# Kernel tuning notes

Hardware: AMD Instinct MI355X
Metric: run time of the kernel (lower is better)

## Reference

```python
import jax, jax.numpy as jnp
import numpy as np

N_CHARS, EMB, HID, T = 256, 512, 2048, 8192


def setup_inputs() -> dict:
    key = jax.random.key(0)
    ks = jax.random.split(key, 12)
    s_in = 1.0 / np.sqrt(EMB + HID)
    s_out = 1.0 / np.sqrt(HID)
    return {
        "input_seq": jax.random.randint(ks[0], (T,), 0, N_CHARS, dtype=jnp.int32),
        "emb": jax.random.normal(ks[1], (N_CHARS, EMB), jnp.float32),
        "W_f": jax.random.uniform(ks[2], (HID, EMB + HID), jnp.float32, -s_in, s_in),
        "b_f": jax.random.uniform(ks[3], (HID,), jnp.float32, -s_in, s_in),
        "W_i": jax.random.uniform(ks[4], (HID, EMB + HID), jnp.float32, -s_in, s_in),
        "b_i": jax.random.uniform(ks[5], (HID,), jnp.float32, -s_in, s_in),
        "W_o": jax.random.uniform(ks[6], (HID, EMB + HID), jnp.float32, -s_in, s_in),
        "b_o": jax.random.uniform(ks[7], (HID,), jnp.float32, -s_in, s_in),
        "W_c": jax.random.uniform(ks[8], (HID, EMB + HID), jnp.float32, -s_in, s_in),
        "b_c": jax.random.uniform(ks[9], (HID,), jnp.float32, -s_in, s_in),
        "W_y": jax.random.uniform(ks[10], (N_CHARS, HID), jnp.float32, -s_out, s_out),
        "b_y": jax.random.uniform(ks[11], (N_CHARS,), jnp.float32, -s_out, s_out),
    }


def reference(input_seq, emb, W_f, b_f, W_i, b_i, W_o, b_o, W_c, b_c, W_y, b_y):
    x = emb[input_seq]  # [T, EMB]
    # Fuse the 4 gate Linears into one stacked GEMM per step (same math).
    W_all = jnp.concatenate([W_f, W_i, W_c, W_o], axis=0)  # [4H, E+H]
    b_all = jnp.concatenate([b_f, b_i, b_c, b_o], axis=0)  # [4H]
    H = b_f.shape[0]

    def step(carry, xt):
        h, c = carry
        z = jnp.concatenate([xt, h])              # [E+H]
        g = W_all @ z + b_all                      # [4H]
        f_t = jax.nn.sigmoid(g[:H])
        i_t = jax.nn.sigmoid(g[H:2 * H])
        c_tilda = jnp.tanh(g[2 * H:3 * H])
        o_t = jax.nn.sigmoid(g[3 * H:])
        c = f_t * c + i_t * c_tilda
        h = o_t * jnp.tanh(c)
        y_t = W_y @ h + b_y                        # [N_CHARS]
        return (h, c), y_t

    h0 = jnp.zeros((H,), x.dtype)
    c0 = jnp.zeros((H,), x.dtype)
    (h, c), y = jax.lax.scan(step, (h0, c0), x)
    return y, h, c
```

## Files before the change

kernel.cpp:

```cpp
#include <hip/hip_runtime.h>
#include <cstdint>

typedef unsigned int uint;
typedef unsigned short ushort;
typedef unsigned char uchar;
typedef unsigned long long u64;
typedef long long i64;

#define TSTEPS 8192
#define HIDDEN 2048
#define EMBDIM 512

#define CAL_MARGIN 1400ull
#define CAL_MINPE  2400ull
#define CAL_MAXPE  5800ull

__device__ __forceinline__ ushort f2bf(float f) {
  uint u = __float_as_uint(f);
  uint r = u + 0x7fffu + ((u >> 16) & 1u);
  return (ushort)(r >> 16);
}
__device__ __forceinline__ float bf2f(ushort h) {
  return __uint_as_float(((uint)h) << 16);
}
__device__ __forceinline__ uint pk2(float a, float b) {
  return (uint)f2bf(a) | ((uint)f2bf(b) << 16);
}

typedef __bf16 bf16x2 __attribute__((ext_vector_type(2)));

__device__ __forceinline__ float dot2bf(uint a, uint b, float acc) {
#if __has_builtin(__builtin_amdgcn_fdot2_f32_bf16)
  return __builtin_amdgcn_fdot2_f32_bf16(__builtin_bit_cast(bf16x2, a),
                                         __builtin_bit_cast(bf16x2, b), acc, false);
#else
  acc += bf2f((ushort)(a & 0xffffu)) * bf2f((ushort)(b & 0xffffu));
  acc += bf2f((ushort)(a >> 16))     * bf2f((ushort)(b >> 16));
  return acc;
#endif
}

__device__ __forceinline__ float sigm(float x)   { return 1.0f / (1.0f + __expf(-x)); }
__device__ __forceinline__ float tanh_f(float x) { return 1.0f - 2.0f / (__expf(2.0f * x) + 1.0f); }

__global__ __launch_bounds__(256) void gx_kernel(
    const float* __restrict__ emb,
    const float* __restrict__ Wf, const float* __restrict__ bf_,
    const float* __restrict__ Wi, const float* __restrict__ bi_,
    const float* __restrict__ Wc, const float* __restrict__ bc_,
    const float* __restrict__ Wo, const float* __restrict__ bo_,
    ushort* __restrict__ gxg)
{
  __shared__ uint4 Wsh4[32 * 64];
  __shared__ uint4 Esh4[16 * 65];
  ushort* W_sh = (ushort*)Wsh4;
  ushort* e_sh = (ushort*)Esh4;
  const int tid = threadIdx.x, bid = blockIdx.x;

  for (int idx = tid; idx < 32 * 512; idx += 256) {
    int lr = idx >> 9, e = idx & 511;
    int gate = lr >> 3, jj = lr & 7;
    const float* Wg = (gate == 0) ? Wf : (gate == 1) ? Wi : (gate == 2) ? Wc : Wo;
    W_sh[lr * 512 + e] = f2bf(Wg[(size_t)(bid * 8 + jj) * 2560 + e]);
  }
  const int lr = tid >> 3, cp = tid & 7;
  const int gate = lr >> 3, jj = lr & 7;
  const float* bg = (gate == 0) ? bf_ : (gate == 1) ? bi_ : (gate == 2) ? bc_ : bo_;
  const float bias = bg[bid * 8 + jj];

  for (int ct = 0; ct < 16; ++ct) {
    __syncthreads();
    for (int idx = tid; idx < 16 * 512; idx += 256) {
      int cc = idx >> 9, e = idx & 511;
      e_sh[cc * 520 + e] = f2bf(emb[(size_t)(ct * 16 + cc) * 512 + e]);
    }
    __syncthreads();
    const uint4* wrow = Wsh4 + lr * 64;
    const uint4* ea = Esh4 + (cp * 2) * 65;
    const uint4* eb = Esh4 + (cp * 2 + 1) * 65;
    float a0 = 0.f, a1 = 0.f;
#pragma unroll 4
    for (int e8 = 0; e8 < 64; ++e8) {
      uint4 wv = wrow[e8], va = ea[e8], vb = eb[e8];
      a0 = dot2bf(wv.x, va.x, a0); a0 = dot2bf(wv.y, va.y, a0);
      a0 = dot2bf(wv.z, va.z, a0); a0 = dot2bf(wv.w, va.w, a0);
      a1 = dot2bf(wv.x, vb.x, a1); a1 = dot2bf(wv.y, vb.y, a1);
      a1 = dot2bf(wv.z, vb.z, a1); a1 = dot2bf(wv.w, vb.w, a1);
    }
    int ch0 = ct * 16 + cp * 2;
    gxg[(size_t)bid * 8192 + ch0 * 32 + lr]       = f2bf(a0 + bias);
    gxg[(size_t)bid * 8192 + (ch0 + 1) * 32 + lr] = f2bf(a1 + bias);
  }
}

__global__ __launch_bounds__(256) void wyb_kernel(const float* __restrict__ Wy,
                                                  ushort* __restrict__ Wyb)
{
  int i = blockIdx.x * 256 + threadIdx.x;
  if (i < 131072) {
    float4 v = ((const float4*)Wy)[i];
    uint2 o; o.x = pk2(v.x, v.y); o.y = pk2(v.z, v.w);
    ((uint2*)Wyb)[i] = o;
  }
}

__global__ __launch_bounds__(1024, 4) void lstm_kernel(
    const int* __restrict__ seq,
    const float* __restrict__ Wf, const float* __restrict__ Wi,
    const float* __restrict__ Wc, const float* __restrict__ Wo,
    const ushort* __restrict__ gxg,
    uint* __restrict__ hist,
    u64* __restrict__ hbuf,
    float* __restrict__ out_h, float* __restrict__ out_c)
{
  __shared__ uint4 hsh4[256];
  __shared__ uint4 gxsh4[1024];
  __shared__ uchar seq_sh[TSTEPS];
  __shared__ float g_sh[32];
  __shared__ float c_sh[8];
  __shared__ u64 sched_last;
  __shared__ u64 sched_pe;

  const int tid = threadIdx.x, bid = blockIdx.x;
  const int w = tid >> 6, g = tid & 63;

  const int lr0 = 2 * w;
  const int gate = lr0 >> 3, jj0 = lr0 & 7;
  const float* Wg = (gate == 0) ? Wf : (gate == 1) ? Wi : (gate == 2) ? Wc : Wo;
  const float* W0 = Wg + (size_t)(bid * 8 + jj0) * 2560 + 512;
  const float* W1 = W0 + 2560;
  uint4 wa[4], wb[4];
#pragma unroll
  for (int i = 0; i < 4; ++i) {
    int col = (i * 64 + g) * 8;
    float4 x0 = *(const float4*)(W0 + col);
    float4 x1 = *(const float4*)(W0 + col + 4);
    wa[i] = make_uint4(pk2(x0.x, x0.y), pk2(x0.z, x0.w), pk2(x1.x, x1.y), pk2(x1.z, x1.w));
    float4 y0 = *(const float4*)(W1 + col);
    float4 y1 = *(const float4*)(W1 + col + 4);
    wb[i] = make_uint4(pk2(y0.x, y0.y), pk2(y0.z, y0.w), pk2(y1.x, y1.y), pk2(y1.z, y1.w));
  }

  gxsh4[tid] = ((const uint4*)(gxg + (size_t)bid * 8192))[tid];
  {
    int4 v0 = ((const int4*)seq)[tid];
    int4 v1 = ((const int4*)seq)[tid + 1024];
    seq_sh[4 * tid + 0] = (uchar)v0.x; seq_sh[4 * tid + 1] = (uchar)v0.y;
    seq_sh[4 * tid + 2] = (uchar)v0.z; seq_sh[4 * tid + 3] = (uchar)v0.w;
    seq_sh[4096 + 4 * tid + 0] = (uchar)v1.x; seq_sh[4096 + 4 * tid + 1] = (uchar)v1.y;
    seq_sh[4096 + 4 * tid + 2] = (uchar)v1.z; seq_sh[4096 + 4 * tid + 3] = (uchar)v1.w;
  }
  if (tid < 256) hsh4[tid] = make_uint4(0u, 0u, 0u, 0u);
  if (tid < 8)  c_sh[tid] = 0.f;
  if (tid == 0) { sched_last = clock64(); sched_pe = 0ull; }
  __syncthreads();

  const ushort* gx_sh = (const ushort*)gxsh4;
  uint* hsh_dw = (uint*)hsh4;
  uint ovsl = 0;

  for (int t = 0; t < TSTEPS; ++t) {
    if (tid == 0) {
      u64 now = clock64();
      u64 raw = now - sched_last;
      sched_last = now;
      if (raw > 4 * CAL_MAXPE) raw = 4 * CAL_MAXPE;
      u64 pe = sched_pe;
      pe = pe - (pe >> 2) + (raw >> 2);
      if (ovsl) pe -= (pe >> 4);
      if (pe > CAL_MAXPE) pe = CAL_MAXPE;
      sched_pe = pe;
    }

    float a0 = 0.f, a1 = 0.f;
#pragma unroll
    for (int i = 0; i < 4; ++i) {
      uint4 hv = hsh4[i * 64 + g];
      a0 = dot2bf(wa[i].x, hv.x, a0); a0 = dot2bf(wa[i].y, hv.y, a0);
      a0 = dot2bf(wa[i].z, hv.z, a0); a0 = dot2bf(wa[i].w, hv.w, a0);
      a1 = dot2bf(wb[i].x, hv.x, a1); a1 = dot2bf(wb[i].y, hv.y, a1);
      a1 = dot2bf(wb[i].z, hv.z, a1); a1 = dot2bf(wb[i].w, hv.w, a1);
    }
    float s0 = __shfl_xor(a0, 32);
    float s1 = __shfl_xor(a1, 32);
    float a = (g < 32) ? (a0 + s0) : (a1 + s1);
    a += __shfl_xor(a, 16); a += __shfl_xor(a, 8);
    a += __shfl_xor(a, 4);  a += __shfl_xor(a, 2); a += __shfl_xor(a, 1);
    if ((g & 31) == 0) g_sh[lr0 + (g >> 5)] = a;
    __syncthreads();

    if (w == 0 && g < 8) {
      const int ch = (int)seq_sh[t];
      const ushort* gx = gx_sh + ch * 32;
      float vf = g_sh[g]      + bf2f(gx[g]);
      float vi = g_sh[8 + g]  + bf2f(gx[8 + g]);
      float vc = g_sh[16 + g] + bf2f(gx[16 + g]);
      float vo = g_sh[24 + g] + bf2f(gx[24 + g]);
      float f_ = sigm(vf), i_ = sigm(vi), ct_ = tanh_f(vc), o_ = sigm(vo);
      float cn = f_ * c_sh[g] + i_ * ct_;
      c_sh[g] = cn;
      float h = o_ * tanh_f(cn);
      uint hb = (uint)f2bf(h);
      uint nb = __shfl_down(hb, 1);
      if ((g & 1) == 0) {
        uint dw = hb | (nb << 16);
        int di = bid * 4 + (g >> 1);
        u64 v = (u64)dw | ((u64)(uint)(t + 1) << 32);
        __hip_atomic_store(hbuf + (size_t)(t & 1) * 1024 + di, v,
                           __ATOMIC_RELAXED, __HIP_MEMORY_SCOPE_AGENT);
        __builtin_nontemporal_store(dw, hist + (size_t)t * 1024 + di);
      }
      if (t == TSTEPS - 1) { out_h[bid * 8 + g] = h; out_c[bid * 8 + g] = cn; }
    }

    if (t < TSTEPS - 1) {
      {
        u64 pe = sched_pe;
        if (pe > CAL_MINPE) {
          u64 tgt = sched_last + pe - CAL_MARGIN;
          while ((i64)(tgt - clock64()) > 0) __builtin_amdgcn_s_sleep(2);
        }
      }
      const u64 want = (u64)(uint)(t + 1);
      const u64* slot = hbuf + (size_t)(t & 1) * 1024 + tid;
      u64 v = __hip_atomic_load(slot, __ATOMIC_RELAXED, __HIP_MEMORY_SCOPE_AGENT);
      ovsl = ((v >> 32) == want) ? 1u : 0u;
      while ((v >> 32) != want) {
        __builtin_amdgcn_s_sleep(2);
        v = __hip_atomic_load(slot, __ATOMIC_RELAXED, __HIP_MEMORY_SCOPE_AGENT);
      }
      hsh_dw[tid] = (uint)v;
    }
    __syncthreads();
  }
}

__global__ __launch_bounds__(256) void y_kernel(
    const ushort* __restrict__ hist,
    const ushort* __restrict__ Wyb,
    const float* __restrict__ by,
    float* __restrict__ y)
{
  __shared__ uint4 hsh4[4096];
  const int tid = threadIdx.x, bid = blockIdx.x;
  const int t0 = bid * 16;
  const uint4* src = (const uint4*)(hist + (size_t)t0 * 2048);
  for (int i = tid; i < 4096; i += 256) hsh4[i] = src[i];
  __syncthreads();
  const int a = tid >> 6, b = tid & 63;
  const int n0 = b * 4;
  float acc[4][4];
#pragma unroll
  for (int i = 0; i < 4; ++i)
#pragma unroll
    for (int j = 0; j < 4; ++j) acc[i][j] = 0.f;
  const uint4* wy = (const uint4*)Wyb;
  for (int k8 = 0; k8 < 256; ++k8) {
    uint4 hv[4];
#pragma unroll
    for (int ti = 0; ti < 4; ++ti) hv[ti] = hsh4[(a + ti * 4) * 256 + k8];
#pragma unroll
    for (int nj = 0; nj < 4; ++nj) {
      uint4 wv = wy[(size_t)(n0 + nj) * 256 + k8];
#pragma unroll
      for (int ti = 0; ti < 4; ++ti) {
        acc[ti][nj] = dot2bf(hv[ti].x, wv.x, acc[ti][nj]);
        acc[ti][nj] = dot2bf(hv[ti].y, wv.y, acc[ti][nj]);
        acc[ti][nj] = dot2bf(hv[ti].z, wv.z, acc[ti][nj]);
        acc[ti][nj] = dot2bf(hv[ti].w, wv.w, acc[ti][nj]);
      }
    }
  }
  float4 bv = *(const float4*)(by + n0);
#pragma unroll
  for (int ti = 0; ti < 4; ++ti) {
    int t = t0 + a + ti * 4;
    float4 o;
    o.x = acc[ti][0] + bv.x; o.y = acc[ti][1] + bv.y;
    o.z = acc[ti][2] + bv.z; o.w = acc[ti][3] + bv.w;
    *(float4*)(y + (size_t)t * 256 + n0) = o;
  }
}

extern "C" void kernel_launch(void* const* d_in, const int* in_sizes, int n_in,
                              void* d_out, int out_size, void* d_ws, size_t ws_size,
                              hipStream_t stream)
{
  const int*   seq = (const int*)d_in[0];
  const float* emb = (const float*)d_in[1];
  const float* Wf  = (const float*)d_in[2];
  const float* bf_ = (const float*)d_in[3];
  const float* Wi  = (const float*)d_in[4];
  const float* bi_ = (const float*)d_in[5];
  const float* Wo  = (const float*)d_in[6];
  const float* bo_ = (const float*)d_in[7];
  const float* Wc  = (const float*)d_in[8];
  const float* bc_ = (const float*)d_in[9];
  const float* Wy  = (const float*)d_in[10];
  const float* by  = (const float*)d_in[11];

  const size_t OFF_GXG  = 0;
  const size_t OFF_HIST = 4194304;
  const size_t OFF_HBUF = OFF_HIST + 33554432;
  const size_t OFF_WYB  = OFF_HBUF + 16384;
  const size_t NEEDED   = OFF_WYB + 1048576;
  if (ws_size < NEEDED) return;

  char* ws = (char*)d_ws;
  ushort* gxg  = (ushort*)(ws + OFF_GXG);
  ushort* hist = (ushort*)(ws + OFF_HIST);
  u64*    hbuf = (u64*)   (ws + OFF_HBUF);
  ushort* Wyb  = (ushort*)(ws + OFF_WYB);

  float* yout  = (float*)d_out;
  float* out_h = yout + (size_t)TSTEPS * 256;
  float* out_c = out_h + HIDDEN;

  hipLaunchKernelGGL(gx_kernel, dim3(256), dim3(256), 0, stream,
                     emb, Wf, bf_, Wi, bi_, Wc, bc_, Wo, bo_, gxg);
  hipLaunchKernelGGL(wyb_kernel, dim3(512), dim3(256), 0, stream, Wy, Wyb);
  hipLaunchKernelGGL(lstm_kernel, dim3(256), dim3(1024), 0, stream,
                     seq, Wf, Wi, Wc, Wo, gxg, (uint*)hist, hbuf,
                     out_h, out_c);
  hipLaunchKernelGGL(y_kernel, dim3(512), dim3(256), 0, stream,
                     hist, Wyb, by, yout);
}
```

Baseline: 17.13 ms.

## Halve persistent LSTM blocks to 128, each computing 16 hidden units

Result: slower. 21.07 ms (+23.0%).

```diff
diff --git a/kernel.cpp b/kernel.cpp
--- a/kernel.cpp
+++ b/kernel.cpp
@@ -10,8 +10,9 @@
 #define TSTEPS 8192
 #define HIDDEN 2048
 #define EMBDIM 512
-
-#define CAL_MARGIN 1400ull
+#define NBLK   128
+
+#define CAL_MARGIN 1800ull
 #define CAL_MINPE  2400ull
 #define CAL_MAXPE  5800ull
 
@@ -114,34 +115,43 @@
     float* __restrict__ out_h, float* __restrict__ out_c)
 {
   __shared__ uint4 hsh4[256];
-  __shared__ uint4 gxsh4[1024];
+  __shared__ uint4 gxsh4[2048];
   __shared__ uchar seq_sh[TSTEPS];
-  __shared__ float g_sh[32];
-  __shared__ float c_sh[8];
+  __shared__ float g_sh[64];
+  __shared__ float c_sh[16];
   __shared__ u64 sched_last;
   __shared__ u64 sched_pe;
 
   const int tid = threadIdx.x, bid = blockIdx.x;
   const int w = tid >> 6, g = tid & 63;
 
-  const int lr0 = 2 * w;
-  const int gate = lr0 >> 3, jj0 = lr0 & 7;
+  const int gate = w >> 2;
+  const int jj0 = (4 * w) & 15;
   const float* Wg = (gate == 0) ? Wf : (gate == 1) ? Wi : (gate == 2) ? Wc : Wo;
-  const float* W0 = Wg + (size_t)(bid * 8 + jj0) * 2560 + 512;
-  const float* W1 = W0 + 2560;
-  uint4 wa[4], wb[4];
-#pragma unroll
-  for (int i = 0; i < 4; ++i) {
-    int col = (i * 64 + g) * 8;
-    float4 x0 = *(const float4*)(W0 + col);
-    float4 x1 = *(const float4*)(W0 + col + 4);
-    wa[i] = make_uint4(pk2(x0.x, x0.y), pk2(x0.z, x0.w), pk2(x1.x, x1.y), pk2(x1.z, x1.w));
-    float4 y0 = *(const float4*)(W1 + col);
-    float4 y1 = *(const float4*)(W1 + col + 4);
-    wb[i] = make_uint4(pk2(y0.x, y0.y), pk2(y0.z, y0.w), pk2(y1.x, y1.y), pk2(y1.z, y1.w));
-  }
-
-  gxsh4[tid] = ((const uint4*)(gxg + (size_t)bid * 8192))[tid];
+  const float* Wr0 = Wg + (size_t)(bid * 16 + jj0) * 2560 + 512;
+  uint4 wreg[4][4];
+#pragma unroll
+  for (int r = 0; r < 4; ++r) {
+    const float* Wr = Wr0 + (size_t)r * 2560;
+#pragma unroll
+    for (int i = 0; i < 4; ++i) {
+      int col = (i * 64 + g) * 8;
+      float4 x0 = *(const float4*)(Wr + col);
+      float4 x1 = *(const float4*)(Wr + col + 4);
+      wreg[r][i] = make_uint4(pk2(x0.x, x0.y), pk2(x0.z, x0.w),
+                              pk2(x1.x, x1.y), pk2(x1.z, x1.w));
+    }
+  }
+
+  {
+    const uint4* g0 = (const uint4*)(gxg + (size_t)(2 * bid) * 8192);
+    const uint4* g1 = (const uint4*)(gxg + (size_t)(2 * bid + 1) * 8192);
+    for (int idx = tid; idx < 2048; idx += 1024) {
+      int ch = idx >> 3, m = idx & 7;
+      const uint4* gsrc = (m & 1) ? g1 : g0;
+      gxsh4[idx] = gsrc[ch * 4 + (m >> 1)];
+    }
+  }
   {
     int4 v0 = ((const int4*)seq)[tid];
     int4 v1 = ((const int4*)seq)[tid + 1024];
@@ -151,7 +161,7 @@
     seq_sh[4096 + 4 * tid + 2] = (uchar)v1.z; seq_sh[4096 + 4 * tid + 3] = (uchar)v1.w;
   }
   if (tid < 256) hsh4[tid] = make_uint4(0u, 0u, 0u, 0u);
-  if (tid < 8)  c_sh[tid] = 0.f;
+  if (tid < 16) c_sh[tid] = 0.f;
   if (tid == 0) { sched_last = clock64(); sched_pe = 0ull; }
   __syncthreads();
 
@@ -172,30 +182,41 @@
       sched_pe = pe;
     }
 
-    float a0 = 0.f, a1 = 0.f;
+    float ac0 = 0.f, ac1 = 0.f, ac2 = 0.f, ac3 = 0.f;
 #pragma unroll
     for (int i = 0; i < 4; ++i) {
       uint4 hv = hsh4[i * 64 + g];
-      a0 = dot2bf(wa[i].x, hv.x, a0); a0 = dot2bf(wa[i].y, hv.y, a0);
-      a0 = dot2bf(wa[i].z, hv.z, a0); a0 = dot2bf(wa[i].w, hv.w, a0);
-      a1 = dot2bf(wb[i].x, hv.x, a1); a1 = dot2bf(wb[i].y, hv.y, a1);
-      a1 = dot2bf(wb[i].z, hv.z, a1); a1 = dot2bf(wb[i].w, hv.w, a1);
-    }
-    float s0 = __shfl_xor(a0, 32);
-    float s1 = __shfl_xor(a1, 32);
-    float a = (g < 32) ? (a0 + s0) : (a1 + s1);
-    a += __shfl_xor(a, 16); a += __shfl_xor(a, 8);
-    a += __shfl_xor(a, 4);  a += __shfl_xor(a, 2); a += __shfl_xor(a, 1);
-    if ((g & 31) == 0) g_sh[lr0 + (g >> 5)] = a;
+      ac0 = dot2bf(wreg[0][i].x, hv.x, ac0); ac0 = dot2bf(wreg[0][i].y, hv.y, ac0);
+      ac0 = dot2bf(wreg[0][i].z, hv.z, ac0); ac0 = dot2bf(wreg[0][i].w, hv.w, ac0);
+      ac1 = dot2bf(wreg[1][i].x, hv.x, ac1); ac1 = dot2bf(wreg[1][i].y, hv.y, ac1);
+      ac1 = dot2bf(wreg[1][i].z, hv.z, ac1); ac1 = dot2bf(wreg[1][i].w, hv.w, ac1);
+      ac2 = dot2bf(wreg[2][i].x, hv.x, ac2); ac2 = dot2bf(wreg[2][i].y, hv.y, ac2);
+      ac2 = dot2bf(wreg[2][i].z, hv.z, ac2); ac2 = dot2bf(wreg[2][i].w, hv.w, ac2);
+      ac3 = dot2bf(wreg[3][i].x, hv.x, ac3); ac3 = dot2bf(wreg[3][i].y, hv.y, ac3);
+      ac3 = dot2bf(wreg[3][i].z, hv.z, ac3); ac3 = dot2bf(wreg[3][i].w, hv.w, ac3);
+    }
+    float s0 = __shfl_xor(ac0, 32), s1 = __shfl_xor(ac1, 32);
+    float s2 = __shfl_xor(ac2, 32), s3 = __shfl_xor(ac3, 32);
+    float a = (g < 32) ? (ac0 + s0) : (ac2 + s2);
+    float b = (g < 32) ? (ac1 + s1) : (ac3 + s3);
+    a += __shfl_xor(a, 16); b += __shfl_xor(b, 16);
+    a += __shfl_xor(a, 8);  b += __shfl_xor(b, 8);
+    a += __shfl_xor(a, 4);  b += __shfl_xor(b, 4);
+    a += __shfl_xor(a, 2);  b += __shfl_xor(b, 2);
+    a += __shfl_xor(a, 1);  b += __shfl_xor(b, 1);
+    if ((g & 31) == 0) {
+      int base = 4 * w + (g >> 5) * 2;
+      g_sh[base] = a; g_sh[base + 1] = b;
+    }
     __syncthreads();
 
-    if (w == 0 && g < 8) {
+    if (w == 0 && g < 16) {
       const int ch = (int)seq_sh[t];
-      const ushort* gx = gx_sh + ch * 32;
+      const ushort* gx = gx_sh + ch * 64;
       float vf = g_sh[g]      + bf2f(gx[g]);
-      float vi = g_sh[8 + g]  + bf2f(gx[8 + g]);
-      float vc = g_sh[16 + g] + bf2f(gx[16 + g]);
-      float vo = g_sh[24 + g] + bf2f(gx[24 + g]);
+      float vi = g_sh[16 + g] + bf2f(gx[16 + g]);
+      float vc = g_sh[32 + g] + bf2f(gx[32 + g]);
+      float vo = g_sh[48 + g] + bf2f(gx[48 + g]);
       float f_ = sigm(vf), i_ = sigm(vi), ct_ = tanh_f(vc), o_ = sigm(vo);
       float cn = f_ * c_sh[g] + i_ * ct_;
       c_sh[g] = cn;
@@ -204,13 +225,13 @@
       uint nb = __shfl_down(hb, 1);
       if ((g & 1) == 0) {
         uint dw = hb | (nb << 16);
-        int di = bid * 4 + (g >> 1);
+        int di = bid * 8 + (g >> 1);
         u64 v = (u64)dw | ((u64)(uint)(t + 1) << 32);
         __hip_atomic_store(hbuf + (size_t)(t & 1) * 1024 + di, v,
                            __ATOMIC_RELAXED, __HIP_MEMORY_SCOPE_AGENT);
         __builtin_nontemporal_store(dw, hist + (size_t)t * 1024 + di);
       }
-      if (t == TSTEPS - 1) { out_h[bid * 8 + g] = h; out_c[bid * 8 + g] = cn; }
+      if (t == TSTEPS - 1) { out_h[bid * 16 + g] = h; out_c[bid * 16 + g] = cn; }
     }
 
     if (t < TSTEPS - 1) {
@@ -226,7 +247,6 @@
       u64 v = __hip_atomic_load(slot, __ATOMIC_RELAXED, __HIP_MEMORY_SCOPE_AGENT);
       ovsl = ((v >> 32) == want) ? 1u : 0u;
       while ((v >> 32) != want) {
-        __builtin_amdgcn_s_sleep(2);
         v = __hip_atomic_load(slot, __ATOMIC_RELAXED, __HIP_MEMORY_SCOPE_AGENT);
       }
       hsh_dw[tid] = (uint)v;
@@ -319,7 +339,7 @@
   hipLaunchKernelGGL(gx_kernel, dim3(256), dim3(256), 0, stream,
                      emb, Wf, bf_, Wi, bi_, Wc, bc_, Wo, bo_, gxg);
   hipLaunchKernelGGL(wyb_kernel, dim3(512), dim3(256), 0, stream, Wy, Wyb);
-  hipLaunchKernelGGL(lstm_kernel, dim3(256), dim3(1024), 0, stream,
+  hipLaunchKernelGGL(lstm_kernel, dim3(NBLK), dim3(1024), 0, stream,
                      seq, Wf, Wi, Wc, Wo, gxg, (uint*)hist, hbuf,
                      out_h, out_c);
   hipLaunchKernelGGL(y_kernel, dim3(512), dim3(256), 0, stream,
```
